# Kernel optimization log

Measured on AMD Instinct MI355X. Metric: run time of the kernel, lower is better.

## Reference

```python
import jax, jax.numpy as jnp
import numpy as np
from jax import lax

DIM = 256
HEADS = 8
EPS = 1e-12  # torch F.normalize eps


def setup_inputs() -> dict:
    key = jax.random.key(0)
    ks = jax.random.split(key, 6)
    b, c, h, w = 2, DIM, 128, 128
    x = jax.random.normal(ks[0], (b, c, h, w), dtype=jnp.float32)
    # qkv 1x1 conv (no bias): weight [3*dim, dim]
    w_qkv = jax.random.normal(ks[1], (3 * c, c), dtype=jnp.float32) * (1.0 / np.sqrt(c))
    # depthwise 3x3 conv, groups = 3*dim: weight [3*dim, 1, 3, 3]
    w_dw = jax.random.normal(ks[2], (3 * c, 1, 3, 3), dtype=jnp.float32) * (1.0 / 3.0)
    # project_out 1x1 conv: [dim, dim]
    w_proj = jax.random.normal(ks[3], (c, c), dtype=jnp.float32) * (1.0 / np.sqrt(c))
    temperature = jnp.ones((HEADS, 1, 1), dtype=jnp.float32)
    a1 = jnp.full((1,), 0.2, dtype=jnp.float32)
    a2 = jnp.full((1,), 0.2, dtype=jnp.float32)
    a3 = jnp.full((1,), 0.2, dtype=jnp.float32)
    a4 = jnp.full((1,), 0.2, dtype=jnp.float32)
    return {"x": x, "w_qkv": w_qkv, "w_dw": w_dw, "w_proj": w_proj,
            "temperature": temperature, "a1": a1, "a2": a2, "a3": a3, "a4": a4}


def _l2norm(t):
    # torch F.normalize(dim=-1): t / max(||t||, eps)
    n = jnp.sqrt(jnp.sum(t * t, axis=-1, keepdims=True))
    return t / jnp.maximum(n, EPS)


def reference(x, w_qkv, w_dw, w_proj, temperature, a1, a2, a3, a4):
    b, c, h, w = x.shape
    heads = temperature.shape[0]
    C = c // heads
    hw = h * w
    # 1x1 conv then depthwise 3x3 conv (groups = 3c)
    qkv = jnp.einsum('oc,bchw->bohw', w_qkv, x)
    qkv = lax.conv_general_dilated(
        qkv, w_dw, window_strides=(1, 1), padding='SAME',
        dimension_numbers=('NCHW', 'OIHW', 'NCHW'), feature_group_count=3 * c)
    q, k, v = jnp.split(qkv, 3, axis=1)
    q = _l2norm(q.reshape(b, heads, C, hw))
    k = _l2norm(k.reshape(b, heads, C, hw))
    v = v.reshape(b, heads, C, hw)
    # channel attention: [b, heads, C, C]
    attn = jnp.einsum('bhcn,bhdn->bhcd', q, k) * temperature
    flat = attn.reshape(b, heads, C * C)
    # share one descending sort across all four top-k passes
    sorted_desc = jnp.sort(flat, axis=-1)[..., ::-1]
    N = C * C
    neg_inf = jnp.asarray(-jnp.inf, dtype=flat.dtype)

    def spar_softmax(topk):
        thresh = sorted_desc[..., topk - 1:topk]  # kth largest value
        masked = jnp.where(flat >= thresh, flat, neg_inf)
        return jax.nn.softmax(masked, axis=-1).reshape(b, heads, C, C)

    s1 = spar_softmax(N * 1 // 2)
    s2 = spar_softmax(N * 2 // 3)
    s3 = spar_softmax(N * 3 // 4)
    s4 = spar_softmax(N * 4 // 5)
    spar = s1 * a1 + s2 * a2 + s3 * a3 + s4 * a4
    out = jnp.einsum('bhcd,bhdn->bhcn', spar, v).reshape(b, c, h, w)
    out = jnp.einsum('oc,bchw->bohw', w_proj, out)
    return out
```

## Files before the change

kernel.cpp:

```cpp
#include <hip/hip_runtime.h>
#include <stdint.h>

#define HW     16384
#define IMGW   128
#define NCH    768
#define DIMC   256
#define NB     2
#define CPH    32

typedef unsigned short u16;
typedef unsigned int   u32;
typedef __attribute__((ext_vector_type(8))) short bf16x8;
typedef __attribute__((ext_vector_type(4))) float f32x4;

__device__ __forceinline__ float bf2f(u16 u) { return __uint_as_float(((u32)u) << 16); }
__device__ __forceinline__ u16 f2bf(float f) {
    u32 u = __float_as_uint(f);
    u += 0x7fffu + ((u >> 16) & 1u);
    return (u16)(u >> 16);
}

#define GLOAD16(gp, lp) __builtin_amdgcn_global_load_lds( \
    (const __attribute__((address_space(1))) void*)(gp),  \
    (__attribute__((address_space(3))) void*)(lp), 16, 0, 0)

__global__ __launch_bounds__(256)
void wsplit(const float* __restrict__ w, u16* __restrict__ wh, u16* __restrict__ wl)
{
    const int idx = blockIdx.x * 256 + threadIdx.x;
    const int m = idx >> 3, s = idx & 7;
    const int p = (m >> 1) & 3;
    #pragma unroll
    for (int u = 0; u < 4; ++u) {
        const int cb = s * 32 + ((u ^ p) << 3);
        u32 hq[4], lq[4];
        #pragma unroll
        for (int e2 = 0; e2 < 4; ++e2) {
            float f0 = w[m * 256 + cb + 2 * e2];
            float f1 = w[m * 256 + cb + 2 * e2 + 1];
            u16 h0 = f2bf(f0); u16 l0 = f2bf(f0 - bf2f(h0));
            u16 h1 = f2bf(f1); u16 l1 = f2bf(f1 - bf2f(h1));
            hq[e2] = (u32)h0 | ((u32)h1 << 16);
            lq[e2] = (u32)l0 | ((u32)l1 << 16);
        }
        size_t rowb = ((size_t)(s * 768 + m)) << 6;
        uint4 hv; hv.x = hq[0]; hv.y = hq[1]; hv.z = hq[2]; hv.w = hq[3];
        uint4 lv; lv.x = lq[0]; lv.y = lq[1]; lv.z = lq[2]; lv.w = lq[3];
        *(uint4*)((char*)wh + rowb + (u << 4)) = hv;
        *(uint4*)((char*)wl + rowb + (u << 4)) = lv;
    }
}

__global__ __launch_bounds__(256)
void transp_split(const float* __restrict__ src, long srcBatch,
                  u16* __restrict__ dsth, u16* __restrict__ dstl)
{
    __shared__ float Xs[64][68];
    const int bz = blockIdx.y;
    const int nt = blockIdx.x & 255;
    const int ct = blockIdx.x >> 8;
    const int n0 = nt * 64, c0 = ct * 64;
    const int t = threadIdx.x;
    const float* xb = src + (size_t)bz * srcBatch;

    #pragma unroll
    for (int it = 0; it < 4; ++it) {
        int cl = (t >> 4) + it * 16;
        int nl4 = (t & 15) << 2;
        float4 v = *(const float4*)(xb + (size_t)(c0 + cl) * HW + n0 + nl4);
        Xs[cl][nl4]     = v.x; Xs[cl][nl4 + 1] = v.y;
        Xs[cl][nl4 + 2] = v.z; Xs[cl][nl4 + 3] = v.w;
    }
    __syncthreads();

    const int nl = t >> 2, u = t & 3;
    const int p = (nl >> 1) & 3;
    #pragma unroll
    for (int sl = 0; sl < 2; ++sl) {
        const int s = (c0 >> 5) + sl;
        const int cb = sl * 32 + ((u ^ p) << 3);
        u32 hq[4], lq[4];
        #pragma unroll
        for (int e2 = 0; e2 < 4; ++e2) {
            float f0 = Xs[cb + 2 * e2][nl];
            float f1 = Xs[cb + 2 * e2 + 1][nl];
            u16 h0 = f2bf(f0); u16 l0 = f2bf(f0 - bf2f(h0));
            u16 h1 = f2bf(f1); u16 l1 = f2bf(f1 - bf2f(h1));
            hq[e2] = (u32)h0 | ((u32)h1 << 16);
            lq[e2] = (u32)l0 | ((u32)l1 << 16);
        }
        size_t rowb = ((size_t)((bz * 8 + s)) * 16384 + n0 + nl) << 6;
        uint4 hv; hv.x = hq[0]; hv.y = hq[1]; hv.z = hq[2]; hv.w = hq[3];
        uint4 lv; lv.x = lq[0]; lv.y = lq[1]; lv.z = lq[2]; lv.w = lq[3];
        *(uint4*)((char*)dsth + rowb + (u << 4)) = hv;
        *(uint4*)((char*)dstl + rowb + (u << 4)) = lv;
    }
}

__global__ __launch_bounds__(256)
void transp_bf(const u16* __restrict__ src, long srcBatch, u16* __restrict__ dsth)
{
    __shared__ u16 Xs[64][66];
    const int bz = blockIdx.y;
    const int nt = blockIdx.x & 255;
    const int ct = blockIdx.x >> 8;
    const int n0 = nt * 64, c0 = ct * 64;
    const int t = threadIdx.x;
    const u16* xb = src + (size_t)bz * srcBatch;

    #pragma unroll
    for (int it = 0; it < 4; ++it) {
        int cl = (t >> 4) + it * 16;
        int nl4 = (t & 15) << 2;
        ushort4 v = *(const ushort4*)(xb + (size_t)(c0 + cl) * HW + n0 + nl4);
        Xs[cl][nl4] = v.x; Xs[cl][nl4 + 1] = v.y;
        Xs[cl][nl4 + 2] = v.z; Xs[cl][nl4 + 3] = v.w;
    }
    __syncthreads();

    const int nl = t >> 2, u = t & 3;
    const int p = (nl >> 1) & 3;
    #pragma unroll
    for (int sl = 0; sl < 2; ++sl) {
        const int s = (c0 >> 5) + sl;
        const int cb = sl * 32 + ((u ^ p) << 3);
        u32 q[4];
        #pragma unroll
        for (int e2 = 0; e2 < 4; ++e2)
            q[e2] = (u32)Xs[cb + 2 * e2][nl] | ((u32)Xs[cb + 2 * e2 + 1][nl] << 16);
        size_t rowb = ((size_t)((bz * 8 + s)) * 16384 + n0 + nl) << 6;
        uint4 hv; hv.x = q[0]; hv.y = q[1]; hv.z = q[2]; hv.w = q[3];
        *(uint4*)((char*)dsth + rowb + (u << 4)) = hv;
    }
}

template<bool FULLB, bool OUTBF16, int MBLKS>
__global__ __launch_bounds__(256, 2)
void gemm_mfma_split(const u16* __restrict__ Ahp, const u16* __restrict__ Alp,
                     const u16* __restrict__ Bhp, const u16* __restrict__ Blp,
                     void* __restrict__ Cp, int aBatch, int aSlice, long cBatch)
{
    constexpr int BUFSZ = FULLB ? 32768 : 24576;
    __shared__ char smem[2 * BUFSZ];

    const int t    = threadIdx.x;
    const int lane = t & 63;
    const int w    = t >> 6;
    const int per = gridDim.x >> 3;
    const int wid = (blockIdx.x & 7) * per + (blockIdx.x >> 3);
    const int nglob = wid / MBLKS;
    const int m0 = (wid % MBLKS) * 128;
    const int bz = nglob >> 7;
    const int n0 = (nglob & 127) * 128;

    const int lrow  = lane >> 2;
    const int lquad = lane & 3;
    const int mh = w >> 1, nh = w & 1;
    const int swz = ((lane & 15) << 6) + ((((lane >> 4) ^ ((lane >> 1) & 3))) << 4);

    f32x4 acc[4][4];
    #pragma unroll
    for (int i = 0; i < 4; ++i)
        #pragma unroll
        for (int j = 0; j < 4; ++j)
            acc[i][j] = (f32x4){0.f, 0.f, 0.f, 0.f};

    auto stage = [&](int buf, int s) {
        const size_t arow0 = (size_t)bz * aBatch + (size_t)s * aSlice + m0;
        const size_t brow0 = ((size_t)(bz * 8 + s)) * 16384 + n0;
        char* base = smem + buf * BUFSZ;
        constexpr int NCHK = FULLB ? 8 : 6;
        #pragma unroll
        for (int i = 0; i < NCHK; ++i) {
            const int tile = i >> 1;
            const int r16  = ((i & 1) << 2) | w;
            char* dst = base + tile * 8192 + r16 * 1024;
            const char* src;
            if (tile == 0)
                src = (const char*)Ahp + ((arow0 + r16 * 16 + lrow) << 6) + (lquad << 4);
            else if (tile == 1)
                src = (const char*)Alp + ((arow0 + r16 * 16 + lrow) << 6) + (lquad << 4);
            else if (tile == 2)
                src = (const char*)Bhp + ((brow0 + r16 * 16 + lrow) << 6) + (lquad << 4);
            else
                src = (const char*)Blp + ((brow0 + r16 * 16 + lrow) << 6) + (lquad << 4);
            GLOAD16(src, dst);
        }
    };

    stage(0, 0);
    __syncthreads();

    #pragma unroll
    for (int s = 0; s < 8; ++s) {
        char* base = smem + (s & 1) * BUFSZ;
        if (s < 7) stage((s + 1) & 1, s + 1);

        bf16x8 ah[4], al[4], bh[4], bl[4];
        #pragma unroll
        for (int f = 0; f < 4; ++f) {
            const int aoff = (mh * 64 + f * 16) * 64 + swz;
            ah[f] = *(const bf16x8*)(base + aoff);
            al[f] = *(const bf16x8*)(base + 8192 + aoff);
            const int boff = (nh * 64 + f * 16) * 64 + swz;
            bh[f] = *(const bf16x8*)(base + 16384 + boff);
            if (FULLB) bl[f] = *(const bf16x8*)(base + 24576 + boff);
        }

        #pragma unroll
        for (int fm = 0; fm < 4; ++fm)
            #pragma unroll
            for (int fn = 0; fn < 4; ++fn) {
                acc[fm][fn] = __builtin_amdgcn_mfma_f32_16x16x32_bf16(ah[fm], bh[fn], acc[fm][fn], 0, 0, 0);
                if (FULLB)
                    acc[fm][fn] = __builtin_amdgcn_mfma_f32_16x16x32_bf16(ah[fm], bl[fn], acc[fm][fn], 0, 0, 0);
                acc[fm][fn] = __builtin_amdgcn_mfma_f32_16x16x32_bf16(al[fm], bh[fn], acc[fm][fn], 0, 0, 0);
            }

        if (s < 7) __syncthreads();
    }

    #pragma unroll
    for (int fm = 0; fm < 4; ++fm) {
        const int mrow0 = m0 + mh * 64 + fm * 16 + ((lane >> 4) << 2);
        #pragma unroll
        for (int fn = 0; fn < 4; ++fn) {
            const int ncol = n0 + nh * 64 + fn * 16 + (lane & 15);
            if (OUTBF16) {
                u16* Cb = (u16*)Cp + (size_t)bz * cBatch;
                #pragma unroll
                for (int r = 0; r < 4; ++r)
                    Cb[(size_t)(mrow0 + r) * HW + ncol] = f2bf(acc[fm][fn][r]);
            } else {
                float* Cb = (float*)Cp + (size_t)bz * cBatch;
                #pragma unroll
                for (int r = 0; r < 4; ++r)
                    Cb[(size_t)(mrow0 + r) * HW + ncol] = acc[fm][fn][r];
            }
        }
    }
}

__global__ __launch_bounds__(256)
void dwconv3(const u16* __restrict__ in, const float* __restrict__ wdw,
             u16* __restrict__ out)
{
    const int p  = blockIdx.y;
    const int t  = threadIdx.x;
    const int r0 = blockIdx.x * 32 + (t >> 5) * 4;
    const int c0 = (t & 31) << 2;

    const u16* plane = in + (size_t)p * HW;
    const float* wp = wdw + (p % NCH) * 9;
    float w[9];
    #pragma unroll
    for (int i = 0; i < 9; ++i) w[i] = wp[i];

    float rv[6][6];
    #pragma unroll
    for (int j = 0; j < 6; ++j) {
        const int ry = r0 - 1 + j;
        if (ry < 0 || ry >= IMGW) {
            #pragma unroll
            for (int k = 0; k < 6; ++k) rv[j][k] = 0.f;
        } else {
            const u16* rp = plane + ry * IMGW;
            ushort4 vm = *(const ushort4*)(rp + c0);
            rv[j][0] = (c0 > 0)   ? bf2f(rp[c0 - 1]) : 0.f;
            rv[j][1] = bf2f(vm.x); rv[j][2] = bf2f(vm.y);
            rv[j][3] = bf2f(vm.z); rv[j][4] = bf2f(vm.w);
            rv[j][5] = (c0 < 124) ? bf2f(rp[c0 + 4]) : 0.f;
        }
    }

    #pragma unroll
    for (int rr = 0; rr < 4; ++rr) {
        float acc[4] = {0.f, 0.f, 0.f, 0.f};
        #pragma unroll
        for (int dy = 0; dy < 3; ++dy) {
            #pragma unroll
            for (int dx = 0; dx < 3; ++dx) {
                float wv = w[dy * 3 + dx];
                #pragma unroll
                for (int q = 0; q < 4; ++q)
                    acc[q] = fmaf(rv[rr + dy][q + dx], wv, acc[q]);
            }
        }
        ushort4 o4;
        o4.x = f2bf(acc[0]); o4.y = f2bf(acc[1]);
        o4.z = f2bf(acc[2]); o4.w = f2bf(acc[3]);
        *(ushort4*)(out + (size_t)p * HW + (r0 + rr) * IMGW + c0) = o4;
    }
}

__global__ __launch_bounds__(256)
void gram_mfma(const u16* __restrict__ dw, float* __restrict__ part,
               float* __restrict__ sumsqp)
{
    __shared__ float pl[4][32][32];
    __shared__ float sl[4][64];
    const int chunk = blockIdx.x;
    const int bh    = blockIdx.y;
    const int bi = bh >> 3, h = bh & 7;
    const u16* qbase = dw + ((size_t)bi * NCH + h * CPH) * HW;
    const u16* kbase = dw + ((size_t)bi * NCH + 256 + h * CPH) * HW;
    const int t = threadIdx.x, lane = t & 63, w = t >> 6;
    const int lr = lane & 15;
    const int lg = lane >> 4;

    f32x4 acc[2][2];
    #pragma unroll
    for (int i = 0; i < 2; ++i)
        #pragma unroll
        for (int j = 0; j < 2; ++j)
            acc[i][j] = (f32x4){0.f, 0.f, 0.f, 0.f};
    float sq[4] = {0.f, 0.f, 0.f, 0.f};

    #pragma unroll
    for (int ks = 0; ks < 4; ++ks) {
        const int nb = chunk * 512 + w * 128 + ks * 32 + lg * 8;
        bf16x8 a0 = *(const bf16x8*)(qbase + (size_t)lr * HW + nb);
        bf16x8 a1 = *(const bf16x8*)(qbase + (size_t)(lr + 16) * HW + nb);
        bf16x8 b0 = *(const bf16x8*)(kbase + (size_t)lr * HW + nb);
        bf16x8 b1 = *(const bf16x8*)(kbase + (size_t)(lr + 16) * HW + nb);
        acc[0][0] = __builtin_amdgcn_mfma_f32_16x16x32_bf16(a0, b0, acc[0][0], 0, 0, 0);
        acc[0][1] = __builtin_amdgcn_mfma_f32_16x16x32_bf16(a0, b1, acc[0][1], 0, 0, 0);
        acc[1][0] = __builtin_amdgcn_mfma_f32_16x16x32_bf16(a1, b0, acc[1][0], 0, 0, 0);
        acc[1][1] = __builtin_amdgcn_mfma_f32_16x16x32_bf16(a1, b1, acc[1][1], 0, 0, 0);
        #pragma unroll
        for (int e = 0; e < 8; ++e) {
            float f0 = bf2f((u16)a0[e]); sq[0] = fmaf(f0, f0, sq[0]);
            float f1 = bf2f((u16)a1[e]); sq[1] = fmaf(f1, f1, sq[1]);
            float f2 = bf2f((u16)b0[e]); sq[2] = fmaf(f2, f2, sq[2]);
            float f3 = bf2f((u16)b1[e]); sq[3] = fmaf(f3, f3, sq[3]);
        }
    }
    #pragma unroll
    for (int i = 0; i < 4; ++i) {
        sq[i] += __shfl_xor(sq[i], 16);
        sq[i] += __shfl_xor(sq[i], 32);
    }
    if (lane < 16) {
        sl[w][lane]      = sq[0];
        sl[w][16 + lane] = sq[1];
        sl[w][32 + lane] = sq[2];
        sl[w][48 + lane] = sq[3];
    }
    #pragma unroll
    for (int qt = 0; qt < 2; ++qt)
        #pragma unroll
        for (int kt = 0; kt < 2; ++kt)
            #pragma unroll
            for (int r = 0; r < 4; ++r)
                pl[w][qt * 16 + lg * 4 + r][kt * 16 + lr] = acc[qt][kt][r];
    __syncthreads();

    #pragma unroll
    for (int i = 0; i < 4; ++i) {
        const int o = i * 256 + t;
        const int qc = o >> 5, kd = o & 31;
        float s = pl[0][qc][kd] + pl[1][qc][kd] + pl[2][qc][kd] + pl[3][qc][kd];
        part[((size_t)chunk * 16 + bh) * 1024 + o] = s;
    }
    if (t < 64) {
        float s = sl[0][t] + sl[1][t] + sl[2][t] + sl[3][t];
        sumsqp[((size_t)chunk * 16 + bh) * 64 + t] = s;
    }
}

__global__ __launch_bounds__(256)
void gram_finish(const float* __restrict__ part, const float* __restrict__ sumsqp,
                 const float* __restrict__ temp, float* __restrict__ attn)
{
    const int idx = blockIdx.x * 256 + threadIdx.x;
    const int bh = idx >> 10;
    const int h = bh & 7;
    const int c = (idx >> 5) & 31, d = idx & 31;
    float s = 0.f, sqq = 0.f, sqk = 0.f;
    #pragma unroll
    for (int ch = 0; ch < 32; ++ch) {
        s   += part[(size_t)ch * 16384 + idx];
        sqq += sumsqp[((size_t)ch * 16 + bh) * 64 + c];
        sqk += sumsqp[((size_t)ch * 16 + bh) * 64 + 32 + d];
    }
    float iq = 1.f / fmaxf(sqrtf(sqq), 1e-12f);
    float ik = 1.f / fmaxf(sqrtf(sqk), 1e-12f);
    attn[idx] = s * iq * ik * temp[h];
}

__global__ __launch_bounds__(1024)
void sparse_softmax(const float* __restrict__ attn, float* __restrict__ spar,
                    const float* __restrict__ a1, const float* __restrict__ a2,
                    const float* __restrict__ a3, const float* __restrict__ a4)
{
    __shared__ float xs[1024];
    __shared__ float red[16 * 4];
    __shared__ float vthr[4];
    __shared__ float msh;
    __shared__ float ssh[4];

    const int bh = blockIdx.x, t = threadIdx.x;
    float x = attn[bh * 1024 + t];
    xs[t] = x;
    __syncthreads();

    int g = 0, e = 0;
    for (int j = 0; j < 1024; ++j) {
        float v = xs[j];
        g += (v > x);
        e += (v == x);
    }
    if (g == 0) msh = x;
    const int topks[4] = {512, 682, 768, 819};
    #pragma unroll
    for (int kk = 0; kk < 4; ++kk)
        if (g <= topks[kk] - 1 && topks[kk] - 1 < g + e) vthr[kk] = x;
    __syncthreads();

    float m  = msh;
    float ex = expf(x - m);
    float v4[4];
    #pragma unroll
    for (int kk = 0; kk < 4; ++kk) v4[kk] = (x >= vthr[kk]) ? ex : 0.f;
    #pragma unroll
    for (int off = 32; off; off >>= 1)
        #pragma unroll
        for (int kk = 0; kk < 4; ++kk) v4[kk] += __shfl_down(v4[kk], off);
    const int lane = t & 63, wid = t >> 6;
    if (lane == 0) {
        #pragma unroll
        for (int kk = 0; kk < 4; ++kk) red[wid * 4 + kk] = v4[kk];
    }
    __syncthreads();
    if (t == 0) {
        float s0 = 0, s1 = 0, s2 = 0, s3 = 0;
        for (int w = 0; w < 16; ++w) {
            s0 += red[w * 4 + 0]; s1 += red[w * 4 + 1];
            s2 += red[w * 4 + 2]; s3 += red[w * 4 + 3];
        }
        ssh[0] = s0; ssh[1] = s1; ssh[2] = s2; ssh[3] = s3;
    }
    __syncthreads();

    float av[4] = {*a1, *a2, *a3, *a4};
    float coef = 0.f;
    #pragma unroll
    for (int kk = 0; kk < 4; ++kk)
        if (x >= vthr[kk]) coef += av[kk] / ssh[kk];
    spar[bh * 1024 + t] = ex * coef;
}

__global__ __launch_bounds__(256)
void build_m2_split(const float* __restrict__ wproj, const float* __restrict__ spar,
                    u16* __restrict__ m2h, u16* __restrict__ m2l)
{
    const int idx = blockIdx.x * 256 + threadIdx.x;
    const int b = idx >> 16, o = (idx >> 8) & 255, hd = idx & 255;
    const int h = hd >> 5, d = hd & 31;
    const float* wrow = wproj + o * 256 + h * CPH;
    const float* sp = spar + (size_t)(b * 8 + h) * 1024 + d;
    float acc = 0.f;
    #pragma unroll 8
    for (int cc = 0; cc < 32; ++cc)
        acc = fmaf(wrow[cc], sp[cc * 32], acc);
    u16 hi = f2bf(acc);
    u16 lo = f2bf(acc - bf2f(hi));
    const int s = hd >> 5, cslot = hd & 31;
    const int qt = cslot >> 3, e = cslot & 7;
    const int p = (o >> 1) & 3;
    size_t pos = ((size_t)(b * 2048 + s * 256 + o) << 5) + ((qt ^ p) << 3) + e;
    m2h[pos] = hi;
    m2l[pos] = lo;
}

extern "C" void kernel_launch(void* const* d_in, const int* in_sizes, int n_in,
                              void* d_out, int out_size, void* d_ws, size_t ws_size,
                              hipStream_t stream)
{
    const float* x      = (const float*)d_in[0];
    const float* w_qkv  = (const float*)d_in[1];
    const float* w_dw   = (const float*)d_in[2];
    const float* w_proj = (const float*)d_in[3];
    const float* temp   = (const float*)d_in[4];
    const float* a1     = (const float*)d_in[5];
    const float* a2     = (const float*)d_in[6];
    const float* a3     = (const float*)d_in[7];
    const float* a4     = (const float*)d_in[8];

    float* ws = (float*)d_ws;
    u16* qkvb = (u16*)ws;
    u16* vth  = (u16*)(ws + 12582912);
    float* sumsqp = ws;
    float* part = ws + 32768;
    float* attn = ws + 32768 + 524288;
    float* spar = attn + 16384;
    u16* m2h = (u16*)(spar + 16384);
    u16* m2l = m2h + 131072;
    float* r1 = ws + (size_t)25165824;
    u16* xth = (u16*)r1;
    u16* xtl = xth + (size_t)8388608;
    u16* whp = xtl + (size_t)8388608;
    u16* wlp = whp + (size_t)196608;
    u16* dwb = (u16*)r1;

    wsplit<<<24, 256, 0, stream>>>(w_qkv, whp, wlp);
    transp_split<<<dim3(1024, 2), 256, 0, stream>>>(x, (long)DIMC * HW, xth, xtl);
    gemm_mfma_split<true, true, 6><<<1536, 256, 0, stream>>>(
        whp, wlp, xth, xtl, qkvb, 0, 768, (long)NCH * HW);
    dwconv3<<<dim3(4, NB * NCH), 256, 0, stream>>>(qkvb, w_dw, dwb);
    transp_bf<<<dim3(1024, 2), 256, 0, stream>>>(
        dwb + (size_t)512 * HW, (long)NCH * HW, vth);
    gram_mfma<<<dim3(32, 16), 256, 0, stream>>>(dwb, part, sumsqp);
    gram_finish<<<64, 256, 0, stream>>>(part, sumsqp, temp, attn);
    sparse_softmax<<<16, 1024, 0, stream>>>(attn, spar, a1, a2, a3, a4);
    build_m2_split<<<512, 256, 0, stream>>>(w_proj, spar, m2h, m2l);
    gemm_mfma_split<false, false, 2><<<512, 256, 0, stream>>>(
        m2h, m2l, vth, nullptr, d_out, 2048, 256, (long)DIMC * HW);
}
```

Before: 148.3 us.

## Drop LDS staging in GEMMs, fuse V dwconv with transpose, merge gram finish into softmax

The split-bf16 GEMM no longer stages tiles in LDS with async global-to-LDS loads and double buffering. Each wave now loads its MFMA fragments straight from global memory, so the XOR swizzle in the packed layouts is removed everywhere. The V-channel depthwise conv is fused with the transpose into a new kernel that writes the n-major layout directly, removing one full-tensor pass. The gram finalisation is folded into the sparse softmax kernel, whose rank-counting loop now reads shared memory as float4. Direct global fragment loads lose the shared reuse across waves and may raise L2 traffic in the large QKV GEMM.

```diff
diff --git a/kernel.cpp b/kernel.cpp
--- a/kernel.cpp
+++ b/kernel.cpp
@@ -20,34 +20,30 @@
     return (u16)(u >> 16);
 }
 
-#define GLOAD16(gp, lp) __builtin_amdgcn_global_load_lds( \
-    (const __attribute__((address_space(1))) void*)(gp),  \
-    (__attribute__((address_space(3))) void*)(lp), 16, 0, 0)
-
 __global__ __launch_bounds__(256)
 void wsplit(const float* __restrict__ w, u16* __restrict__ wh, u16* __restrict__ wl)
 {
     const int idx = blockIdx.x * 256 + threadIdx.x;
     const int m = idx >> 3, s = idx & 7;
-    const int p = (m >> 1) & 3;
-    #pragma unroll
-    for (int u = 0; u < 4; ++u) {
-        const int cb = s * 32 + ((u ^ p) << 3);
+    const float* src = w + m * 256 + s * 32;
+    u16* dh = wh + ((size_t)(s * 768 + m)) * 32;
+    u16* dl = wl + ((size_t)(s * 768 + m)) * 32;
+    #pragma unroll
+    for (int e = 0; e < 4; ++e) {
         u32 hq[4], lq[4];
         #pragma unroll
         for (int e2 = 0; e2 < 4; ++e2) {
-            float f0 = w[m * 256 + cb + 2 * e2];
-            float f1 = w[m * 256 + cb + 2 * e2 + 1];
+            float f0 = src[e * 8 + 2 * e2];
+            float f1 = src[e * 8 + 2 * e2 + 1];
             u16 h0 = f2bf(f0); u16 l0 = f2bf(f0 - bf2f(h0));
             u16 h1 = f2bf(f1); u16 l1 = f2bf(f1 - bf2f(h1));
             hq[e2] = (u32)h0 | ((u32)h1 << 16);
             lq[e2] = (u32)l0 | ((u32)l1 << 16);
         }
-        size_t rowb = ((size_t)(s * 768 + m)) << 6;
-        uint4 hv; hv.x = hq[0]; hv.y = hq[1]; hv.z = hq[2]; hv.w = hq[3];
-        uint4 lv; lv.x = lq[0]; lv.y = lq[1]; lv.z = lq[2]; lv.w = lq[3];
-        *(uint4*)((char*)wh + rowb + (u << 4)) = hv;
-        *(uint4*)((char*)wl + rowb + (u << 4)) = lv;
+        uint4 hv = {hq[0], hq[1], hq[2], hq[3]};
+        uint4 lv = {lq[0], lq[1], lq[2], lq[3]};
+        *(uint4*)(dh + e * 8) = hv;
+        *(uint4*)(dl + e * 8) = lv;
     }
 }
 
@@ -74,11 +70,10 @@
     __syncthreads();
 
     const int nl = t >> 2, u = t & 3;
-    const int p = (nl >> 1) & 3;
     #pragma unroll
     for (int sl = 0; sl < 2; ++sl) {
         const int s = (c0 >> 5) + sl;
-        const int cb = sl * 32 + ((u ^ p) << 3);
+        const int cb = sl * 32 + (u << 3);
         u32 hq[4], lq[4];
         #pragma unroll
         for (int e2 = 0; e2 < 4; ++e2) {
@@ -90,59 +85,19 @@
             lq[e2] = (u32)l0 | ((u32)l1 << 16);
         }
         size_t rowb = ((size_t)((bz * 8 + s)) * 16384 + n0 + nl) << 6;
-        uint4 hv; hv.x = hq[0]; hv.y = hq[1]; hv.z = hq[2]; hv.w = hq[3];
-        uint4 lv; lv.x = lq[0]; lv.y = lq[1]; lv.z = lq[2]; lv.w = lq[3];
+        uint4 hv = {hq[0], hq[1], hq[2], hq[3]};
+        uint4 lv = {lq[0], lq[1], lq[2], lq[3]};
         *(uint4*)((char*)dsth + rowb + (u << 4)) = hv;
         *(uint4*)((char*)dstl + rowb + (u << 4)) = lv;
     }
 }
 
-__global__ __launch_bounds__(256)
-void transp_bf(const u16* __restrict__ src, long srcBatch, u16* __restrict__ dsth)
-{
-    __shared__ u16 Xs[64][66];
-    const int bz = blockIdx.y;
-    const int nt = blockIdx.x & 255;
-    const int ct = blockIdx.x >> 8;
-    const int n0 = nt * 64, c0 = ct * 64;
-    const int t = threadIdx.x;
-    const u16* xb = src + (size_t)bz * srcBatch;
-
-    #pragma unroll
-    for (int it = 0; it < 4; ++it) {
-        int cl = (t >> 4) + it * 16;
-        int nl4 = (t & 15) << 2;
-        ushort4 v = *(const ushort4*)(xb + (size_t)(c0 + cl) * HW + n0 + nl4);
-        Xs[cl][nl4] = v.x; Xs[cl][nl4 + 1] = v.y;
-        Xs[cl][nl4 + 2] = v.z; Xs[cl][nl4 + 3] = v.w;
-    }
-    __syncthreads();
-
-    const int nl = t >> 2, u = t & 3;
-    const int p = (nl >> 1) & 3;
-    #pragma unroll
-    for (int sl = 0; sl < 2; ++sl) {
-        const int s = (c0 >> 5) + sl;
-        const int cb = sl * 32 + ((u ^ p) << 3);
-        u32 q[4];
-        #pragma unroll
-        for (int e2 = 0; e2 < 4; ++e2)
-            q[e2] = (u32)Xs[cb + 2 * e2][nl] | ((u32)Xs[cb + 2 * e2 + 1][nl] << 16);
-        size_t rowb = ((size_t)((bz * 8 + s)) * 16384 + n0 + nl) << 6;
-        uint4 hv; hv.x = q[0]; hv.y = q[1]; hv.z = q[2]; hv.w = q[3];
-        *(uint4*)((char*)dsth + rowb + (u << 4)) = hv;
-    }
-}
-
 template<bool FULLB, bool OUTBF16, int MBLKS>
 __global__ __launch_bounds__(256, 2)
-void gemm_mfma_split(const u16* __restrict__ Ahp, const u16* __restrict__ Alp,
-                     const u16* __restrict__ Bhp, const u16* __restrict__ Blp,
-                     void* __restrict__ Cp, int aBatch, int aSlice, long cBatch)
-{
-    constexpr int BUFSZ = FULLB ? 32768 : 24576;
-    __shared__ char smem[2 * BUFSZ];
-
+void gemm_direct(const u16* __restrict__ Ahp, const u16* __restrict__ Alp,
+                 const u16* __restrict__ Bhp, const u16* __restrict__ Blp,
+                 void* __restrict__ Cp, int aBatch, int aSlice, long cBatch)
+{
     const int t    = threadIdx.x;
     const int lane = t & 63;
     const int w    = t >> 6;
@@ -153,10 +108,9 @@
     const int bz = nglob >> 7;
     const int n0 = (nglob & 127) * 128;
 
-    const int lrow  = lane >> 2;
-    const int lquad = lane & 3;
     const int mh = w >> 1, nh = w & 1;
-    const int swz = ((lane & 15) << 6) + ((((lane >> 4) ^ ((lane >> 1) & 3))) << 4);
+    const int lr = lane & 15;
+    const int lq = lane >> 4;
 
     f32x4 acc[4][4];
     #pragma unroll
@@ -165,48 +119,19 @@
         for (int j = 0; j < 4; ++j)
             acc[i][j] = (f32x4){0.f, 0.f, 0.f, 0.f};
 
-    auto stage = [&](int buf, int s) {
-        const size_t arow0 = (size_t)bz * aBatch + (size_t)s * aSlice + m0;
-        const size_t brow0 = ((size_t)(bz * 8 + s)) * 16384 + n0;
-        char* base = smem + buf * BUFSZ;
-        constexpr int NCHK = FULLB ? 8 : 6;
-        #pragma unroll
-        for (int i = 0; i < NCHK; ++i) {
-            const int tile = i >> 1;
-            const int r16  = ((i & 1) << 2) | w;
-            char* dst = base + tile * 8192 + r16 * 1024;
-            const char* src;
-            if (tile == 0)
-                src = (const char*)Ahp + ((arow0 + r16 * 16 + lrow) << 6) + (lquad << 4);
-            else if (tile == 1)
-                src = (const char*)Alp + ((arow0 + r16 * 16 + lrow) << 6) + (lquad << 4);
-            else if (tile == 2)
-                src = (const char*)Bhp + ((brow0 + r16 * 16 + lrow) << 6) + (lquad << 4);
-            else
-                src = (const char*)Blp + ((brow0 + r16 * 16 + lrow) << 6) + (lquad << 4);
-            GLOAD16(src, dst);
-        }
-    };
-
-    stage(0, 0);
-    __syncthreads();
-
-    #pragma unroll
     for (int s = 0; s < 8; ++s) {
-        char* base = smem + (s & 1) * BUFSZ;
-        if (s < 7) stage((s + 1) & 1, s + 1);
-
+        const size_t arow = (size_t)bz * aBatch + (size_t)s * aSlice + m0 + mh * 64;
+        const size_t brow = ((size_t)(bz * 8 + s)) * 16384 + n0 + nh * 64;
         bf16x8 ah[4], al[4], bh[4], bl[4];
         #pragma unroll
         for (int f = 0; f < 4; ++f) {
-            const int aoff = (mh * 64 + f * 16) * 64 + swz;
-            ah[f] = *(const bf16x8*)(base + aoff);
-            al[f] = *(const bf16x8*)(base + 8192 + aoff);
-            const int boff = (nh * 64 + f * 16) * 64 + swz;
-            bh[f] = *(const bf16x8*)(base + 16384 + boff);
-            if (FULLB) bl[f] = *(const bf16x8*)(base + 24576 + boff);
-        }
-
+            const size_t ao = (arow + f * 16 + lr) * 32 + lq * 8;
+            ah[f] = *(const bf16x8*)(Ahp + ao);
+            al[f] = *(const bf16x8*)(Alp + ao);
+            const size_t bo = (brow + f * 16 + lr) * 32 + lq * 8;
+            bh[f] = *(const bf16x8*)(Bhp + bo);
+            if (FULLB) bl[f] = *(const bf16x8*)(Blp + bo);
+        }
         #pragma unroll
         for (int fm = 0; fm < 4; ++fm)
             #pragma unroll
@@ -216,16 +141,14 @@
                     acc[fm][fn] = __builtin_amdgcn_mfma_f32_16x16x32_bf16(ah[fm], bl[fn], acc[fm][fn], 0, 0, 0);
                 acc[fm][fn] = __builtin_amdgcn_mfma_f32_16x16x32_bf16(al[fm], bh[fn], acc[fm][fn], 0, 0, 0);
             }
-
-        if (s < 7) __syncthreads();
     }
 
     #pragma unroll
     for (int fm = 0; fm < 4; ++fm) {
-        const int mrow0 = m0 + mh * 64 + fm * 16 + ((lane >> 4) << 2);
+        const int mrow0 = m0 + mh * 64 + fm * 16 + (lq << 2);
         #pragma unroll
         for (int fn = 0; fn < 4; ++fn) {
-            const int ncol = n0 + nh * 64 + fn * 16 + (lane & 15);
+            const int ncol = n0 + nh * 64 + fn * 16 + lr;
             if (OUTBF16) {
                 u16* Cb = (u16*)Cp + (size_t)bz * cBatch;
                 #pragma unroll
@@ -245,13 +168,15 @@
 void dwconv3(const u16* __restrict__ in, const float* __restrict__ wdw,
              u16* __restrict__ out)
 {
-    const int p  = blockIdx.y;
+    const int y  = blockIdx.y;
+    const int bi = y >> 9, ch = y & 511;
+    const size_t p = (size_t)bi * NCH + ch;
     const int t  = threadIdx.x;
     const int r0 = blockIdx.x * 32 + (t >> 5) * 4;
     const int c0 = (t & 31) << 2;
 
-    const u16* plane = in + (size_t)p * HW;
-    const float* wp = wdw + (p % NCH) * 9;
+    const u16* plane = in + p * HW;
+    const float* wp = wdw + ch * 9;
     float w[9];
     #pragma unroll
     for (int i = 0; i < 9; ++i) w[i] = wp[i];
@@ -289,8 +214,75 @@
         ushort4 o4;
         o4.x = f2bf(acc[0]); o4.y = f2bf(acc[1]);
         o4.z = f2bf(acc[2]); o4.w = f2bf(acc[3]);
-        *(ushort4*)(out + (size_t)p * HW + (r0 + rr) * IMGW + c0) = o4;
-    }
+        *(ushort4*)(out + p * HW + (r0 + rr) * IMGW + c0) = o4;
+    }
+}
+
+__global__ __launch_bounds__(256)
+void dwconv_v(const u16* __restrict__ qkvb, const float* __restrict__ wdw,
+              u16* __restrict__ vth)
+{
+    __shared__ u16 Lout[256][40];
+    const int rp = blockIdx.x;
+    const int s  = blockIdx.y;
+    const int bz = blockIdx.z;
+    const int t  = threadIdx.x;
+    const int ch = t >> 3;
+    const int cg = t & 7;
+    const int r0 = rp * 2;
+    const int c0 = cg * 16;
+    const int chg = 512 + s * 32 + ch;
+    const u16* plane = qkvb + ((size_t)bz * NCH + chg) * HW;
+    const float* wp = wdw + chg * 9;
+    float w[9];
+    #pragma unroll
+    for (int i = 0; i < 9; ++i) w[i] = wp[i];
+
+    float rv[4][18];
+    #pragma unroll
+    for (int j = 0; j < 4; ++j) {
+        const int ry = r0 - 1 + j;
+        if (ry < 0 || ry >= IMGW) {
+            #pragma unroll
+            for (int k = 0; k < 18; ++k) rv[j][k] = 0.f;
+        } else {
+            const u16* rw = plane + ry * IMGW;
+            bf16x8 v0 = *(const bf16x8*)(rw + c0);
+            bf16x8 v1 = *(const bf16x8*)(rw + c0 + 8);
+            rv[j][0] = (c0 > 0) ? bf2f(rw[c0 - 1]) : 0.f;
+            #pragma unroll
+            for (int e = 0; e < 8; ++e) {
+                rv[j][1 + e] = bf2f((u16)v0[e]);
+                rv[j][9 + e] = bf2f((u16)v1[e]);
+            }
+            rv[j][17] = (c0 < 112) ? bf2f(rw[c0 + 16]) : 0.f;
+        }
+    }
+
+    #pragma unroll
+    for (int rr = 0; rr < 2; ++rr) {
+        float acc[16];
+        #pragma unroll
+        for (int q = 0; q < 16; ++q) acc[q] = 0.f;
+        #pragma unroll
+        for (int dy = 0; dy < 3; ++dy)
+            #pragma unroll
+            for (int dx = 0; dx < 3; ++dx) {
+                float wv = w[dy * 3 + dx];
+                #pragma unroll
+                for (int q = 0; q < 16; ++q)
+                    acc[q] = fmaf(rv[rr + dy][q + dx], wv, acc[q]);
+            }
+        #pragma unroll
+        for (int q = 0; q < 16; ++q)
+            Lout[rr * 128 + c0 + q][ch] = f2bf(acc[q]);
+    }
+    __syncthreads();
+
+    u16* dst = vth + (((size_t)(bz * 8 + s)) * 16384 + rp * 256 + t) * 32;
+    #pragma unroll
+    for (int e = 0; e < 4; ++e)
+        *(uint4*)(dst + e * 8) = *(const uint4*)(&Lout[t][e * 8]);
 }
 
 __global__ __launch_bounds__(256)
@@ -368,30 +360,11 @@
     }
 }
 
-__global__ __launch_bounds__(256)
-void gram_finish(const float* __restrict__ part, const float* __restrict__ sumsqp,
-                 const float* __restrict__ temp, float* __restrict__ attn)
-{
-    const int idx = blockIdx.x * 256 + threadIdx.x;
-    const int bh = idx >> 10;
-    const int h = bh & 7;
-    const int c = (idx >> 5) & 31, d = idx & 31;
-    float s = 0.f, sqq = 0.f, sqk = 0.f;
-    #pragma unroll
-    for (int ch = 0; ch < 32; ++ch) {
-        s   += part[(size_t)ch * 16384 + idx];
-        sqq += sumsqp[((size_t)ch * 16 + bh) * 64 + c];
-        sqk += sumsqp[((size_t)ch * 16 + bh) * 64 + 32 + d];
-    }
-    float iq = 1.f / fmaxf(sqrtf(sqq), 1e-12f);
-    float ik = 1.f / fmaxf(sqrtf(sqk), 1e-12f);
-    attn[idx] = s * iq * ik * temp[h];
-}
-
 __global__ __launch_bounds__(1024)
-void sparse_softmax(const float* __restrict__ attn, float* __restrict__ spar,
-                    const float* __restrict__ a1, const float* __restrict__ a2,
-                    const float* __restrict__ a3, const float* __restrict__ a4)
+void softfin(const float* __restrict__ part, const float* __restrict__ sumsqp,
+             const float* __restrict__ temp, float* __restrict__ spar,
+             const float* __restrict__ a1, const float* __restrict__ a2,
+             const float* __restrict__ a3, const float* __restrict__ a4)
 {
     __shared__ float xs[1024];
     __shared__ float red[16 * 4];
@@ -400,15 +373,29 @@
     __shared__ float ssh[4];
 
     const int bh = blockIdx.x, t = threadIdx.x;
-    float x = attn[bh * 1024 + t];
+    const int h = bh & 7;
+    const int c = t >> 5, d = t & 31;
+    const int idx = bh * 1024 + t;
+
+    float s = 0.f, sqq = 0.f, sqk = 0.f;
+    #pragma unroll
+    for (int ch = 0; ch < 32; ++ch) {
+        s   += part[(size_t)ch * 16384 + idx];
+        sqq += sumsqp[((size_t)ch * 16 + bh) * 64 + c];
+        sqk += sumsqp[((size_t)ch * 16 + bh) * 64 + 32 + d];
+    }
+    float iq = 1.f / fmaxf(sqrtf(sqq), 1e-12f);
+    float ik = 1.f / fmaxf(sqrtf(sqk), 1e-12f);
+    float x = s * iq * ik * temp[h];
     xs[t] = x;
     __syncthreads();
 
     int g = 0, e = 0;
-    for (int j = 0; j < 1024; ++j) {
-        float v = xs[j];
-        g += (v > x);
-        e += (v == x);
+    const float4* xs4 = (const float4*)xs;
+    for (int j = 0; j < 256; ++j) {
+        float4 v = xs4[j];
+        g += (v.x > x) + (v.y > x) + (v.z > x) + (v.w > x);
+        e += (v.x == x) + (v.y == x) + (v.z == x) + (v.w == x);
     }
     if (g == 0) msh = x;
     const int topks[4] = {512, 682, 768, 819};
@@ -434,9 +421,9 @@
     __syncthreads();
     if (t == 0) {
         float s0 = 0, s1 = 0, s2 = 0, s3 = 0;
-        for (int w = 0; w < 16; ++w) {
-            s0 += red[w * 4 + 0]; s1 += red[w * 4 + 1];
-            s2 += red[w * 4 + 2]; s3 += red[w * 4 + 3];
+        for (int ww = 0; ww < 16; ++ww) {
+            s0 += red[ww * 4 + 0]; s1 += red[ww * 4 + 1];
+            s2 += red[ww * 4 + 2]; s3 += red[ww * 4 + 3];
         }
         ssh[0] = s0; ssh[1] = s1; ssh[2] = s2; ssh[3] = s3;
     }
@@ -466,9 +453,7 @@
     u16 hi = f2bf(acc);
     u16 lo = f2bf(acc - bf2f(hi));
     const int s = hd >> 5, cslot = hd & 31;
-    const int qt = cslot >> 3, e = cslot & 7;
-    const int p = (o >> 1) & 3;
-    size_t pos = ((size_t)(b * 2048 + s * 256 + o) << 5) + ((qt ^ p) << 3) + e;
+    size_t pos = ((size_t)(b * 2048 + s * 256 + o)) * 32 + cslot;
     m2h[pos] = hi;
     m2l[pos] = lo;
 }
@@ -492,8 +477,7 @@
     u16* vth  = (u16*)(ws + 12582912);
     float* sumsqp = ws;
     float* part = ws + 32768;
-    float* attn = ws + 32768 + 524288;
-    float* spar = attn + 16384;
+    float* spar = ws + 32768 + 524288;
     u16* m2h = (u16*)(spar + 16384);
     u16* m2l = m2h + 131072;
     float* r1 = ws + (size_t)25165824;
@@ -505,15 +489,13 @@
 
     wsplit<<<24, 256, 0, stream>>>(w_qkv, whp, wlp);
     transp_split<<<dim3(1024, 2), 256, 0, stream>>>(x, (long)DIMC * HW, xth, xtl);
-    gemm_mfma_split<true, true, 6><<<1536, 256, 0, stream>>>(
+    gemm_direct<true, true, 6><<<1536, 256, 0, stream>>>(
         whp, wlp, xth, xtl, qkvb, 0, 768, (long)NCH * HW);
-    dwconv3<<<dim3(4, NB * NCH), 256, 0, stream>>>(qkvb, w_dw, dwb);
-    transp_bf<<<dim3(1024, 2), 256, 0, stream>>>(
-        dwb + (size_t)512 * HW, (long)NCH * HW, vth);
+    dwconv3<<<dim3(4, NB * 512), 256, 0, stream>>>(qkvb, w_dw, dwb);
+    dwconv_v<<<dim3(64, 8, NB), 256, 0, stream>>>(qkvb, w_dw, vth);
     gram_mfma<<<dim3(32, 16), 256, 0, stream>>>(dwb, part, sumsqp);
-    gram_finish<<<64, 256, 0, stream>>>(part, sumsqp, temp, attn);
-    sparse_softmax<<<16, 1024, 0, stream>>>(attn, spar, a1, a2, a3, a4);
+    softfin<<<16, 1024, 0, stream>>>(part, sumsqp, temp, spar, a1, a2, a3, a4);
     build_m2_split<<<512, 256, 0, stream>>>(w_proj, spar, m2h, m2l);
-    gemm_mfma_split<false, false, 2><<<512, 256, 0, stream>>>(
+    gemm_direct<false, false, 2><<<512, 256, 0, stream>>>(
         m2h, m2l, vth, nullptr, d_out, 2048, 256, (long)DIMC * HW);
 }
```

Measured after the change: 170.5 us. 15.0% more time.
